# Kernel optimization log

Hardware: AMD Instinct MI355X
Metric: run time of the kernel (lower is better)

Reference implementation:

```python
import jax, jax.numpy as jnp
import numpy as np

N, E, F_IN, H, MH, C, G = 100000, 3200000, 128, 32, 64, 10, 64

def _seg_sum(data, ids, num):
    return jax.ops.segment_sum(data, ids, num_segments=num)

def gcn_conv(x, row, col, ew, W, b, n):
    # PyG GCNConv: linear first, then self-loops + symmetric edge-weight norm + scatter-add
    h = x @ W  # [N, H]
    loop = jnp.arange(n)
    r = jnp.concatenate([row, loop])
    c = jnp.concatenate([col, loop])
    w = jnp.concatenate([ew, jnp.ones((n,), dtype=ew.dtype)])
    deg = _seg_sum(w, c, n)
    dinv = jnp.where(deg > 0, jax.lax.rsqrt(deg), 0.0)
    norm = dinv[r] * w * dinv[c]  # [E+N]
    out = _seg_sum(norm[:, None] * h[r], c, n)  # scatter to targets
    return out + b

def setup_inputs():
    key = jax.random.key(0)
    ks = jax.random.split(key, 16)
    inp = {
        "x": jax.random.normal(ks[0], (N, F_IN), dtype=jnp.float32),
        "edge_index": jax.random.randint(ks[1], (2, E), 0, N, dtype=jnp.int64),
        "edge_weight": jax.random.uniform(ks[2], (E,), dtype=jnp.float32),
        "batch": jnp.sort(jax.random.randint(ks[3], (N,), 0, G, dtype=jnp.int64)),
    }
    def lin(k, i, o):
        s = 1.0 / np.sqrt(i)
        k1, k2 = jax.random.split(k)
        return (jax.random.uniform(k1, (i, o), minval=-s, maxval=s, dtype=jnp.float32),
                jax.random.uniform(k2, (o,), minval=-s, maxval=s, dtype=jnp.float32))
    inp["W1"], inp["b1"] = lin(ks[4], F_IN, H)
    inp["W2"], inp["b2"] = lin(ks[5], H, H)
    inp["W3"], inp["b3"] = lin(ks[6], H, H)
    inp["Wm0"], inp["bm0"] = lin(ks[7], H, MH)
    inp["Wm1"], inp["bm1"] = lin(ks[8], MH, MH)
    inp["Wout"], inp["bout"] = lin(ks[9], MH, C)
    return inp

def reference(x, edge_index, edge_weight, batch, W1, b1, W2, b2, W3, b3, Wm0, bm0, Wm1, bm1, Wout, bout):
    row, col = edge_index[0], edge_index[1]
    h = jax.nn.relu(gcn_conv(x, row, col, edge_weight, W1, b1, N))
    h = jax.nn.relu(gcn_conv(h, row, col, edge_weight, W2, b2, N))
    h = gcn_conv(h, row, col, edge_weight, W3, b3, N)
    # global mean pool over graphs
    sums = _seg_sum(h, batch, G)
    counts = _seg_sum(jnp.ones((N,), dtype=h.dtype), batch, G)
    g = sums / jnp.maximum(counts, 1.0)[:, None]
    # dropout p=0.5 is identity at inference (training=False)
    g = jax.nn.relu(g @ Wm0 + bm0)
    g = jax.nn.relu(g @ Wm1 + bm1)
    return g @ Wout + bout
```

## Files before the change

kernel.cpp:

```cpp
#include <hip/hip_runtime.h>

#define NN 100000
#define NE 3200000
#define FIN 128
#define HID 32
#define MH  64
#define NC  10
#define NG  64
#define NBKT 782
#define NBLK 512
#define EPB  (NE / NBLK)
#define SCANL (NBKT * NBLK)
#define SRCMASK 0x1FFFF
#define BCAP 5120

typedef float floatx2 __attribute__((ext_vector_type(2)));

__global__ __launch_bounds__(1024)
void hist_bkt(const int* __restrict__ ei, int* __restrict__ cnt2) {
    __shared__ int h[NBKT];
    int tid = threadIdx.x, blk = blockIdx.x;
    for (int b = tid; b < NBKT; b += 1024) h[b] = 0;
    __syncthreads();
    int base = blk * EPB;
    for (int i = tid; i < EPB; i += 1024)
        atomicAdd(&h[ei[NE + base + i] >> 7], 1);
    __syncthreads();
    for (int b = tid; b < NBKT; b += 1024) cnt2[b * NBLK + blk] = h[b];
}

__global__ void scan_block(const int* __restrict__ in, int* __restrict__ out,
                           int* __restrict__ bsum, int n) {
    __shared__ int lds[256];
    int tid = threadIdx.x;
    int base = blockIdx.x * 1024 + tid * 4;
    int v0 = 0, v1 = 0, v2 = 0, v3 = 0;
    if (base + 0 < n) v0 = in[base + 0];
    if (base + 1 < n) v1 = in[base + 1];
    if (base + 2 < n) v2 = in[base + 2];
    if (base + 3 < n) v3 = in[base + 3];
    int s = v0 + v1 + v2 + v3;
    lds[tid] = s;
    __syncthreads();
    for (int off = 1; off < 256; off <<= 1) {
        int val = (tid >= off) ? lds[tid - off] : 0;
        __syncthreads();
        lds[tid] += val;
        __syncthreads();
    }
    int excl = lds[tid] - s;
    if (tid == 255) bsum[blockIdx.x] = lds[255];
    if (base + 0 < n) out[base + 0] = excl;
    if (base + 1 < n) out[base + 1] = excl + v0;
    if (base + 2 < n) out[base + 2] = excl + v0 + v1;
    if (base + 3 < n) out[base + 3] = excl + v0 + v1 + v2;
}

__global__ void scan_top(int* __restrict__ bsum, int nb, float* __restrict__ sc) {
    int lane = threadIdx.x;
    for (int i = lane; i < NG * HID + NG; i += 64) sc[i] = 0.0f;
    int carry = 0;
    for (int base = 0; base < nb; base += 64) {
        int i = base + lane;
        int orig = (i < nb) ? bsum[i] : 0;
        int v = orig;
#pragma unroll
        for (int off = 1; off < 64; off <<= 1) {
            int t = __shfl_up(v, off, 64);
            if (lane >= off) v += t;
        }
        if (i < nb) bsum[i] = carry + v - orig;
        carry += __shfl(v, 63, 64);
    }
}

__global__ void scan_add(int* __restrict__ data, const int* __restrict__ bsum, int n) {
    int i = blockIdx.x * 256 + threadIdx.x;
    if (i < n) data[i] += bsum[i >> 10];
}

__global__ __launch_bounds__(1024)
void scatter_bkt(const int* __restrict__ ei, const float* __restrict__ ew,
                 const int* __restrict__ cnt2, const int* __restrict__ scanned,
                 int2* __restrict__ tre) {
    __shared__ int2 pay[EPB];
    __shared__ int scur[NBKT];
    __shared__ int hexc[NBKT];
    __shared__ int gbase[NBKT];
    int tid = threadIdx.x, blk = blockIdx.x;
    int myh = 0;
    if (tid < NBKT) {
        myh = cnt2[tid * NBLK + blk];
        gbase[tid] = scanned[tid * NBLK + blk];
        scur[tid] = myh;
    }
    __syncthreads();
    for (int off = 1; off < NBKT; off <<= 1) {
        int v = (tid < NBKT && tid >= off) ? scur[tid - off] : 0;
        __syncthreads();
        if (tid < NBKT) scur[tid] += v;
        __syncthreads();
    }
    if (tid < NBKT) { int ex = scur[tid] - myh; hexc[tid] = ex; scur[tid] = ex; }
    __syncthreads();
    int base = blk * EPB;
    for (int i = tid; i < EPB; i += 1024) {
        int e = base + i;
        int c = ei[NE + e];
        int r = ei[e];
        unsigned int wb = __float_as_uint(ew[e]);
        int b = c >> 7;
        int j = atomicAdd(&scur[b], 1);
        pay[j] = make_int2(r | ((c & 127) << 17) | ((b & 0xFF) << 24),
                           (int)((wb & ~3u) | ((unsigned)b >> 8)));
    }
    __syncthreads();
    for (int j = tid; j < EPB; j += 1024) {
        int2 q = pay[j];
        int b = (int)((((unsigned)q.y & 3u) << 8) | (((unsigned)q.x >> 24) & 0xFFu));
        int pos = gbase[b] + (j - hexc[b]);
        tre[pos] = make_int2(q.x & 0x00FFFFFF, q.y & ~3);
    }
}

__global__ __launch_bounds__(512)
void sort_k(const int2* __restrict__ tre, const int* __restrict__ scanned,
            unsigned int* __restrict__ srn4, int* __restrict__ rowptr,
            float* __restrict__ dinv) {
    __shared__ int2 ed[BCAP];
    __shared__ int h[128];
    __shared__ float dw[128];
    __shared__ int cur[128];
    int b = blockIdx.x, tid = threadIdx.x;
    int base = scanned[b * NBLK];
    int end = (b == NBKT - 1) ? NE : scanned[(b + 1) * NBLK];
    int n = end - base;
    bool staged = (n <= BCAP);
    if (tid < 128) { h[tid] = 0; dw[tid] = 0.f; }
    __syncthreads();
    for (int i = tid; i < n; i += 512) {
        int2 q = tre[base + i];
        if (staged) ed[i] = q;
        int key = (q.x >> 17) & 127;
        atomicAdd(&h[key], 1);
        atomicAdd(&dw[key], __int_as_float(q.y));
    }
    __syncthreads();
    if (tid < 64) {
        int lane = tid;
        int carry = 0;
#pragma unroll
        for (int c = 0; c < 2; ++c) {
            int idx = c * 64 + lane;
            int hv = h[idx];
            int v = hv;
#pragma unroll
            for (int off = 1; off < 64; off <<= 1) {
                int t = __shfl_up(v, off, 64);
                if (lane >= off) v += t;
            }
            cur[idx] = base + carry + v - hv;
            int node = b * 128 + idx;
            if (node < NN) {
                rowptr[node] = base + carry + v;
                dinv[node] = rsqrtf(1.0f + dw[idx]);
            }
            carry += __shfl(v, 63, 64);
        }
    }
    __syncthreads();
    for (int i = tid; i < n; i += 512) {
        int2 q = staged ? ed[i] : tre[base + i];
        int key = (q.x >> 17) & 127;
        int pos = atomicAdd(&cur[key], 1);
        unsigned int wb = (unsigned)q.y;
        wb += 0x7FFFu + ((wb >> 16) & 1u);
        srn4[pos] = (unsigned)(q.x & SRCMASK) | (((wb >> 16) & 0x7FFFu) << 17);
    }
}

template <int IN_DIM, bool RELU_IN>
__global__ __launch_bounds__(256)
void linear_k(const float* __restrict__ in, const float* __restrict__ W,
              const float* __restrict__ dinv, unsigned int* __restrict__ tmp8) {
    constexpr int J4 = IN_DIM / 4;
    constexpr int XSS = J4 + 1;
    __shared__ float4 xs[64 * XSS];
    __shared__ float4 wp[IN_DIM * 8];
    int tid = threadIdx.x;
    for (int idx = tid; idx < IN_DIM * 8; idx += 256) {
        int j = idx >> 3, kg = idx & 7;
        const float* wr = W + j * 32 + kg * 4;
        wp[idx] = make_float4(wr[0], wr[1], wr[2], wr[3]);
    }
    int rbase = blockIdx.x * 64;
    const float4* in4 = (const float4*)in;
    for (int idx = tid; idx < 64 * J4; idx += 256) {
        int row = idx / J4, j4 = idx % J4;
        int grow = rbase + row;
        float4 v = (grow < NN) ? in4[(size_t)grow * J4 + j4]
                               : make_float4(0.f, 0.f, 0.f, 0.f);
        if (RELU_IN) {
            v.x = fmaxf(v.x, 0.f); v.y = fmaxf(v.y, 0.f);
            v.z = fmaxf(v.z, 0.f); v.w = fmaxf(v.w, 0.f);
        }
        xs[row * XSS + j4] = v;
    }
    __syncthreads();
    int kg = tid & 7;
    int rp = tid >> 3;
    int r0 = rbase + 2 * rp;
    if (r0 >= NN) return;
    const float4* x0 = &xs[(2 * rp) * XSS];
    const float4* x1 = &xs[(2 * rp + 1) * XSS];
    float a00 = 0, a01 = 0, a02 = 0, a03 = 0;
    float a10 = 0, a11 = 0, a12 = 0, a13 = 0;
#pragma unroll
    for (int j4 = 0; j4 < J4; ++j4) {
        float4 v0 = x0[j4], v1 = x1[j4];
        const float4* wj = &wp[j4 * 4 * 8 + kg];
        float4 w0 = wj[0], w1 = wj[8], w2 = wj[16], w3 = wj[24];
#define LSTEP(VX0, VX1, W4) \
        a00 = fmaf(VX0, W4.x, a00); a01 = fmaf(VX0, W4.y, a01); \
        a02 = fmaf(VX0, W4.z, a02); a03 = fmaf(VX0, W4.w, a03); \
        a10 = fmaf(VX1, W4.x, a10); a11 = fmaf(VX1, W4.y, a11); \
        a12 = fmaf(VX1, W4.z, a12); a13 = fmaf(VX1, W4.w, a13);
        LSTEP(v0.x, v1.x, w0)
        LSTEP(v0.y, v1.y, w1)
        LSTEP(v0.z, v1.z, w2)
        LSTEP(v0.w, v1.w, w3)
#undef LSTEP
    }
    float d0 = dinv[r0], d1 = dinv[r0 + 1];
    a00 *= d0; a01 *= d0; a02 *= d0; a03 *= d0;
    a10 *= d1; a11 *= d1; a12 *= d1; a13 *= d1;
    int q0 = __builtin_amdgcn_cvt_pk_fp8_f32(a00, a01, 0, false);
    q0 = __builtin_amdgcn_cvt_pk_fp8_f32(a02, a03, q0, true);
    int q1 = __builtin_amdgcn_cvt_pk_fp8_f32(a10, a11, 0, false);
    q1 = __builtin_amdgcn_cvt_pk_fp8_f32(a12, a13, q1, true);
    tmp8[r0 * 8 + kg] = (unsigned int)q0;
    tmp8[(r0 + 1) * 8 + kg] = (unsigned int)q1;
}

#define AGG_BODY \
    int lane = threadIdx.x & 63; \
    int g = lane >> 3; \
    int q = lane & 7; \
    int end = rowptr[wid]; \
    int start = (wid == 0) ? 0 : rowptr[wid - 1]; \
    float a0 = 0, a1 = 0, a2 = 0, a3 = 0; \
    float b0 = 0, b1 = 0, b2 = 0, b3 = 0; \
    int e = start + g; \
    for (; e + 24 < end; e += 32) { \
        unsigned int p0 = srn4[e]; \
        unsigned int p1 = srn4[e + 8]; \
        unsigned int p2 = srn4[e + 16]; \
        unsigned int p3 = srn4[e + 24]; \
        unsigned int u0 = tmp8[(size_t)(p0 & SRCMASK) * 8 + q]; \
        unsigned int u1 = tmp8[(size_t)(p1 & SRCMASK) * 8 + q]; \
        unsigned int u2 = tmp8[(size_t)(p2 & SRCMASK) * 8 + q]; \
        unsigned int u3 = tmp8[(size_t)(p3 & SRCMASK) * 8 + q]; \
        float w0 = __uint_as_float((p0 >> 1) & 0x7FFF0000u); \
        float w1 = __uint_as_float((p1 >> 1) & 0x7FFF0000u); \
        float w2 = __uint_as_float((p2 >> 1) & 0x7FFF0000u); \
        float w3 = __uint_as_float((p3 >> 1) & 0x7FFF0000u); \
        floatx2 lo, hi; \
        lo = __builtin_amdgcn_cvt_pk_f32_fp8(u0, false); \
        hi = __builtin_amdgcn_cvt_pk_f32_fp8(u0, true); \
        a0 = fmaf(w0, lo.x, a0); a1 = fmaf(w0, lo.y, a1); \
        a2 = fmaf(w0, hi.x, a2); a3 = fmaf(w0, hi.y, a3); \
        lo = __builtin_amdgcn_cvt_pk_f32_fp8(u1, false); \
        hi = __builtin_amdgcn_cvt_pk_f32_fp8(u1, true); \
        b0 = fmaf(w1, lo.x, b0); b1 = fmaf(w1, lo.y, b1); \
        b2 = fmaf(w1, hi.x, b2); b3 = fmaf(w1, hi.y, b3); \
        lo = __builtin_amdgcn_cvt_pk_f32_fp8(u2, false); \
        hi = __builtin_amdgcn_cvt_pk_f32_fp8(u2, true); \
        a0 = fmaf(w2, lo.x, a0); a1 = fmaf(w2, lo.y, a1); \
        a2 = fmaf(w2, hi.x, a2); a3 = fmaf(w2, hi.y, a3); \
        lo = __builtin_amdgcn_cvt_pk_f32_fp8(u3, false); \
        hi = __builtin_amdgcn_cvt_pk_f32_fp8(u3, true); \
        b0 = fmaf(w3, lo.x, b0); b1 = fmaf(w3, lo.y, b1); \
        b2 = fmaf(w3, hi.x, b2); b3 = fmaf(w3, hi.y, b3); \
    } \
    for (; e < end; e += 8) { \
        unsigned int p = srn4[e]; \
        unsigned int u = tmp8[(size_t)(p & SRCMASK) * 8 + q]; \
        float w = __uint_as_float((p >> 1) & 0x7FFF0000u); \
        floatx2 lo = __builtin_amdgcn_cvt_pk_f32_fp8(u, false); \
        floatx2 hi = __builtin_amdgcn_cvt_pk_f32_fp8(u, true); \
        a0 = fmaf(w, lo.x, a0); a1 = fmaf(w, lo.y, a1); \
        a2 = fmaf(w, hi.x, a2); a3 = fmaf(w, hi.y, a3); \
    } \
    a0 += b0; a1 += b1; a2 += b2; a3 += b3; \
    a0 += __shfl_xor(a0, 8, 64); a1 += __shfl_xor(a1, 8, 64); \
    a2 += __shfl_xor(a2, 8, 64); a3 += __shfl_xor(a3, 8, 64); \
    a0 += __shfl_xor(a0, 16, 64); a1 += __shfl_xor(a1, 16, 64); \
    a2 += __shfl_xor(a2, 16, 64); a3 += __shfl_xor(a3, 16, 64); \
    a0 += __shfl_xor(a0, 32, 64); a1 += __shfl_xor(a1, 32, 64); \
    a2 += __shfl_xor(a2, 32, 64); a3 += __shfl_xor(a3, 32, 64);

__global__ void aggregate(const unsigned int* __restrict__ srn4,
                          const int* __restrict__ rowptr,
                          const float* __restrict__ dinv,
                          const float* __restrict__ bias,
                          const unsigned int* __restrict__ tmp8,
                          float* __restrict__ h) {
    int wid = (blockIdx.x * 256 + threadIdx.x) >> 6;
    if (wid >= NN) return;
    AGG_BODY
    if (g == 0) {
        float d = dinv[wid];
        unsigned int sv = tmp8[(size_t)wid * 8 + q];
        floatx2 slo = __builtin_amdgcn_cvt_pk_f32_fp8(sv, false);
        floatx2 shi = __builtin_amdgcn_cvt_pk_f32_fp8(sv, true);
        float4 bq = ((const float4*)bias)[q];
        float4 o;
        o.x = bq.x + d * (slo.x + a0);
        o.y = bq.y + d * (slo.y + a1);
        o.z = bq.z + d * (shi.x + a2);
        o.w = bq.w + d * (shi.y + a3);
        ((float4*)(h + (size_t)wid * HID))[q] = o;
    }
}

__global__ void agg_lin(const unsigned int* __restrict__ srn4,
                        const int* __restrict__ rowptr,
                        const float* __restrict__ dinv,
                        const float* __restrict__ bias,
                        const float* __restrict__ Wn,
                        const unsigned int* __restrict__ tmp8,
                        unsigned int* __restrict__ tmp8_out) {
    __shared__ float hrow[4][HID];
    int wid = (blockIdx.x * 256 + threadIdx.x) >> 6;
    if (wid >= NN) return;
    int wv = threadIdx.x >> 6;
    AGG_BODY
    float d = dinv[wid];
    if (g == 0) {
        unsigned int sv = tmp8[(size_t)wid * 8 + q];
        floatx2 slo = __builtin_amdgcn_cvt_pk_f32_fp8(sv, false);
        floatx2 shi = __builtin_amdgcn_cvt_pk_f32_fp8(sv, true);
        float4 bq = ((const float4*)bias)[q];
        float4 o;
        o.x = fmaxf(bq.x + d * (slo.x + a0), 0.f);
        o.y = fmaxf(bq.y + d * (slo.y + a1), 0.f);
        o.z = fmaxf(bq.z + d * (shi.x + a2), 0.f);
        o.w = fmaxf(bq.w + d * (shi.y + a3), 0.f);
        *((float4*)&hrow[wv][4 * q]) = o;
    }
    int j = lane & 31, half = lane >> 5;
    const float* hr = hrow[wv];
    const float* wc = Wn + j;
    float y = 0.f;
#pragma unroll
    for (int k = 0; k < 16; ++k) {
        int kk = half * 16 + k;
        y = fmaf(hr[kk], wc[kk * 32], y);
    }
    y += __shfl_xor(y, 32, 64);
    y *= d;
    float y1 = __shfl_down(y, 1, 64);
    float y2 = __shfl_down(y, 2, 64);
    float y3 = __shfl_down(y, 3, 64);
    if (half == 0 && (j & 3) == 0) {
        int w0 = __builtin_amdgcn_cvt_pk_fp8_f32(y, y1, 0, false);
        w0 = __builtin_amdgcn_cvt_pk_fp8_f32(y2, y3, w0, true);
        tmp8_out[wid * 8 + (j >> 2)] = (unsigned int)w0;
    }
}

__global__ void pool_k(const float* __restrict__ h, const int* __restrict__ batch,
                       float* __restrict__ sums, float* __restrict__ counts) {
    int t = blockIdx.x * 256 + threadIdx.x;
    int chunk = t >> 5, k = t & 31;
    int n0 = chunk * 32;
    if (n0 >= NN) return;
    int n1 = min(n0 + 32, NN);
    int g = batch[n0];
    float acc = 0.f, cacc = 0.f;
    for (int i = n0; i < n1; ++i) {
        int gi = batch[i];
        if (gi != g) {
            atomicAdd(&sums[g * HID + k], acc);
            if (k == 0) atomicAdd(&counts[g], cacc);
            g = gi; acc = 0.f; cacc = 0.f;
        }
        acc += h[(size_t)i * HID + k];
        cacc += 1.f;
    }
    atomicAdd(&sums[g * HID + k], acc);
    if (k == 0) atomicAdd(&counts[g], cacc);
}

__global__ __launch_bounds__(64)
void mlp_k(const float* __restrict__ sums, const float* __restrict__ counts,
           const float* __restrict__ Wm0, const float* __restrict__ bm0,
           const float* __restrict__ Wm1, const float* __restrict__ bm1,
           const float* __restrict__ Wout, const float* __restrict__ bout,
           float* __restrict__ out) {
    __shared__ float g0[HID];
    __shared__ float g1[MH];
    __shared__ float g2[MH];
    int g = blockIdx.x;
    int k = threadIdx.x;
    if (k < HID) g0[k] = sums[g * HID + k] / fmaxf(counts[g], 1.0f);
    __syncthreads();
    float acc = bm0[k];
#pragma unroll
    for (int j = 0; j < HID; ++j) acc = fmaf(g0[j], Wm0[j * MH + k], acc);
    g1[k] = fmaxf(acc, 0.f);
    __syncthreads();
    float acc2 = bm1[k];
#pragma unroll
    for (int j = 0; j < MH; ++j) acc2 = fmaf(g1[j], Wm1[j * MH + k], acc2);
    g2[k] = fmaxf(acc2, 0.f);
    __syncthreads();
    if (k < NC) {
        float acc3 = bout[k];
#pragma unroll
        for (int j = 0; j < MH; ++j) acc3 = fmaf(g2[j], Wout[j * NC + k], acc3);
        out[g * NC + k] = acc3;
    }
}

extern "C" void kernel_launch(void* const* d_in, const int* in_sizes, int n_in,
                              void* d_out, int out_size, void* d_ws, size_t ws_size,
                              hipStream_t stream) {
    const float* x    = (const float*)d_in[0];
    const int*   ei   = (const int*)d_in[1];
    const float* ew   = (const float*)d_in[2];
    const int*   batch= (const int*)d_in[3];
    const float* W1   = (const float*)d_in[4];
    const float* b1   = (const float*)d_in[5];
    const float* W2   = (const float*)d_in[6];
    const float* b2   = (const float*)d_in[7];
    const float* W3   = (const float*)d_in[8];
    const float* b3   = (const float*)d_in[9];
    const float* Wm0  = (const float*)d_in[10];
    const float* bm0  = (const float*)d_in[11];
    const float* Wm1  = (const float*)d_in[12];
    const float* bm1  = (const float*)d_in[13];
    const float* Wout = (const float*)d_in[14];
    const float* bout = (const float*)d_in[15];
    float* out = (float*)d_out;

    char* p = (char*)d_ws;
    unsigned int* srn4 = (unsigned int*)p; p += sizeof(unsigned int) * (size_t)NE;
    char*  S   = p;                      p += 12 * (size_t)NE;
    int2*  tre = (int2*)S;
    int*   cnt2    = (int*)(S + sizeof(int2) * (size_t)NE);
    int*   scanned = cnt2 + SCANL;
    unsigned int* tmp8  = (unsigned int*)S;
    unsigned int* tmp8b = tmp8 + (size_t)NN * 8;
    float* hA  = (float*)(S + 2 * (size_t)NN * HID);
    int*   bsum    = (int*)p;            p += sizeof(int) * 512;
    float* dinv    = (float*)p;          p += sizeof(float) * NN;
    int*   rowptr  = (int*)p;            p += sizeof(int) * NN;
    float* sums    = (float*)p;          p += sizeof(float) * NG * HID;
    float* counts  = (float*)p;

    dim3 blk(256);
    const int NB_SCAN = (SCANL + 1023) / 1024;
    const int NB_LIN = (NN + 63) / 64;

    hist_bkt<<<NBLK, 1024, 0, stream>>>(ei, cnt2);
    scan_block<<<NB_SCAN, blk, 0, stream>>>(cnt2, scanned, bsum, SCANL);
    scan_top<<<1, 64, 0, stream>>>(bsum, NB_SCAN, sums);
    scan_add<<<(SCANL + 255) / 256, blk, 0, stream>>>(scanned, bsum, SCANL);
    scatter_bkt<<<NBLK, 1024, 0, stream>>>(ei, ew, cnt2, scanned, tre);
    sort_k<<<NBKT, 512, 0, stream>>>(tre, scanned, srn4, rowptr, dinv);

    linear_k<FIN, false><<<NB_LIN, blk, 0, stream>>>(x, W1, dinv, tmp8);
    agg_lin<<<25000, blk, 0, stream>>>(srn4, rowptr, dinv, b1, W2, tmp8, tmp8b);
    agg_lin<<<25000, blk, 0, stream>>>(srn4, rowptr, dinv, b2, W3, tmp8b, tmp8);
    aggregate<<<25000, blk, 0, stream>>>(srn4, rowptr, dinv, b3, tmp8, hA);

    pool_k<<<391, blk, 0, stream>>>(hA, batch, sums, counts);
    mlp_k<<<NG, 64, 0, stream>>>(sums, counts, Wm0, bm0, Wm1, bm1, Wout, bout, out);
}
```

Before: 404.6 us.

## Fuse final aggregation with mean-pool and use packed float2 accumulation

Merges the last GCN aggregation with the global mean-pool kernel. Each block accumulates per-graph sums in shared memory when all four nodes share a graph, and otherwise does global atomics. This removes the hA write/read round trip and one launch. The aggregation core now uses packed float2 FMAs with byte-offset address math, and agg_lin loads its hidden row as float4 vectors. The trade-off is extra atomics and a block sync in the fused kernel.

After: 1.110 ms. 2.74x slower.

```diff
diff --git a/kernel.cpp b/kernel.cpp
--- a/kernel.cpp
+++ b/kernel.cpp
@@ -242,72 +242,84 @@
     tmp8[(r0 + 1) * 8 + kg] = (unsigned int)q1;
 }
 
-#define AGG_BODY \
-    int lane = threadIdx.x & 63; \
-    int g = lane >> 3; \
-    int q = lane & 7; \
-    int end = rowptr[wid]; \
-    int start = (wid == 0) ? 0 : rowptr[wid - 1]; \
-    float a0 = 0, a1 = 0, a2 = 0, a3 = 0; \
-    float b0 = 0, b1 = 0, b2 = 0, b3 = 0; \
-    int e = start + g; \
-    for (; e + 24 < end; e += 32) { \
-        unsigned int p0 = srn4[e]; \
-        unsigned int p1 = srn4[e + 8]; \
-        unsigned int p2 = srn4[e + 16]; \
-        unsigned int p3 = srn4[e + 24]; \
-        unsigned int u0 = tmp8[(size_t)(p0 & SRCMASK) * 8 + q]; \
-        unsigned int u1 = tmp8[(size_t)(p1 & SRCMASK) * 8 + q]; \
-        unsigned int u2 = tmp8[(size_t)(p2 & SRCMASK) * 8 + q]; \
-        unsigned int u3 = tmp8[(size_t)(p3 & SRCMASK) * 8 + q]; \
-        float w0 = __uint_as_float((p0 >> 1) & 0x7FFF0000u); \
-        float w1 = __uint_as_float((p1 >> 1) & 0x7FFF0000u); \
-        float w2 = __uint_as_float((p2 >> 1) & 0x7FFF0000u); \
-        float w3 = __uint_as_float((p3 >> 1) & 0x7FFF0000u); \
-        floatx2 lo, hi; \
-        lo = __builtin_amdgcn_cvt_pk_f32_fp8(u0, false); \
-        hi = __builtin_amdgcn_cvt_pk_f32_fp8(u0, true); \
-        a0 = fmaf(w0, lo.x, a0); a1 = fmaf(w0, lo.y, a1); \
-        a2 = fmaf(w0, hi.x, a2); a3 = fmaf(w0, hi.y, a3); \
-        lo = __builtin_amdgcn_cvt_pk_f32_fp8(u1, false); \
-        hi = __builtin_amdgcn_cvt_pk_f32_fp8(u1, true); \
-        b0 = fmaf(w1, lo.x, b0); b1 = fmaf(w1, lo.y, b1); \
-        b2 = fmaf(w1, hi.x, b2); b3 = fmaf(w1, hi.y, b3); \
-        lo = __builtin_amdgcn_cvt_pk_f32_fp8(u2, false); \
-        hi = __builtin_amdgcn_cvt_pk_f32_fp8(u2, true); \
-        a0 = fmaf(w2, lo.x, a0); a1 = fmaf(w2, lo.y, a1); \
-        a2 = fmaf(w2, hi.x, a2); a3 = fmaf(w2, hi.y, a3); \
-        lo = __builtin_amdgcn_cvt_pk_f32_fp8(u3, false); \
-        hi = __builtin_amdgcn_cvt_pk_f32_fp8(u3, true); \
-        b0 = fmaf(w3, lo.x, b0); b1 = fmaf(w3, lo.y, b1); \
-        b2 = fmaf(w3, hi.x, b2); b3 = fmaf(w3, hi.y, b3); \
-    } \
-    for (; e < end; e += 8) { \
-        unsigned int p = srn4[e]; \
-        unsigned int u = tmp8[(size_t)(p & SRCMASK) * 8 + q]; \
-        float w = __uint_as_float((p >> 1) & 0x7FFF0000u); \
-        floatx2 lo = __builtin_amdgcn_cvt_pk_f32_fp8(u, false); \
-        floatx2 hi = __builtin_amdgcn_cvt_pk_f32_fp8(u, true); \
-        a0 = fmaf(w, lo.x, a0); a1 = fmaf(w, lo.y, a1); \
-        a2 = fmaf(w, hi.x, a2); a3 = fmaf(w, hi.y, a3); \
-    } \
-    a0 += b0; a1 += b1; a2 += b2; a3 += b3; \
-    a0 += __shfl_xor(a0, 8, 64); a1 += __shfl_xor(a1, 8, 64); \
-    a2 += __shfl_xor(a2, 8, 64); a3 += __shfl_xor(a3, 8, 64); \
-    a0 += __shfl_xor(a0, 16, 64); a1 += __shfl_xor(a1, 16, 64); \
-    a2 += __shfl_xor(a2, 16, 64); a3 += __shfl_xor(a3, 16, 64); \
-    a0 += __shfl_xor(a0, 32, 64); a1 += __shfl_xor(a1, 32, 64); \
+__device__ __forceinline__ float4 agg_core(const unsigned int* __restrict__ srn4,
+                                           const int* __restrict__ rowptr,
+                                           const unsigned int* __restrict__ tmp8,
+                                           int wid, int g, int q) {
+    unsigned int qb = (unsigned int)q * 4u;
+    const char* t8 = (const char*)tmp8;
+    int end = rowptr[wid];
+    int start = (wid == 0) ? 0 : rowptr[wid - 1];
+    floatx2 a01 = {0.f, 0.f}, a23 = {0.f, 0.f};
+    floatx2 c01 = {0.f, 0.f}, c23 = {0.f, 0.f};
+    int e = start + g;
+    for (; e + 24 < end; e += 32) {
+        unsigned int p0 = srn4[e];
+        unsigned int p1 = srn4[e + 8];
+        unsigned int p2 = srn4[e + 16];
+        unsigned int p3 = srn4[e + 24];
+        unsigned int u0 = *(const unsigned int*)(t8 + (((p0 & SRCMASK) << 5) | qb));
+        unsigned int u1 = *(const unsigned int*)(t8 + (((p1 & SRCMASK) << 5) | qb));
+        unsigned int u2 = *(const unsigned int*)(t8 + (((p2 & SRCMASK) << 5) | qb));
+        unsigned int u3 = *(const unsigned int*)(t8 + (((p3 & SRCMASK) << 5) | qb));
+        float w0 = __uint_as_float((p0 >> 1) & 0x7FFF0000u);
+        float w1 = __uint_as_float((p1 >> 1) & 0x7FFF0000u);
+        float w2 = __uint_as_float((p2 >> 1) & 0x7FFF0000u);
+        float w3 = __uint_as_float((p3 >> 1) & 0x7FFF0000u);
+        floatx2 lo, hi;
+        lo = __builtin_amdgcn_cvt_pk_f32_fp8(u0, false);
+        hi = __builtin_amdgcn_cvt_pk_f32_fp8(u0, true);
+        a01 += lo * w0; a23 += hi * w0;
+        lo = __builtin_amdgcn_cvt_pk_f32_fp8(u1, false);
+        hi = __builtin_amdgcn_cvt_pk_f32_fp8(u1, true);
+        c01 += lo * w1; c23 += hi * w1;
+        lo = __builtin_amdgcn_cvt_pk_f32_fp8(u2, false);
+        hi = __builtin_amdgcn_cvt_pk_f32_fp8(u2, true);
+        a01 += lo * w2; a23 += hi * w2;
+        lo = __builtin_amdgcn_cvt_pk_f32_fp8(u3, false);
+        hi = __builtin_amdgcn_cvt_pk_f32_fp8(u3, true);
+        c01 += lo * w3; c23 += hi * w3;
+    }
+    for (; e < end; e += 8) {
+        unsigned int p = srn4[e];
+        unsigned int u = *(const unsigned int*)(t8 + (((p & SRCMASK) << 5) | qb));
+        float w = __uint_as_float((p >> 1) & 0x7FFF0000u);
+        floatx2 lo = __builtin_amdgcn_cvt_pk_f32_fp8(u, false);
+        floatx2 hi = __builtin_amdgcn_cvt_pk_f32_fp8(u, true);
+        a01 += lo * w; a23 += hi * w;
+    }
+    a01 += c01; a23 += c23;
+    float a0 = a01.x, a1 = a01.y, a2 = a23.x, a3 = a23.y;
+    a0 += __shfl_xor(a0, 8, 64);  a1 += __shfl_xor(a1, 8, 64);
+    a2 += __shfl_xor(a2, 8, 64);  a3 += __shfl_xor(a3, 8, 64);
+    a0 += __shfl_xor(a0, 16, 64); a1 += __shfl_xor(a1, 16, 64);
+    a2 += __shfl_xor(a2, 16, 64); a3 += __shfl_xor(a3, 16, 64);
+    a0 += __shfl_xor(a0, 32, 64); a1 += __shfl_xor(a1, 32, 64);
     a2 += __shfl_xor(a2, 32, 64); a3 += __shfl_xor(a3, 32, 64);
-
-__global__ void aggregate(const unsigned int* __restrict__ srn4,
-                          const int* __restrict__ rowptr,
-                          const float* __restrict__ dinv,
-                          const float* __restrict__ bias,
-                          const unsigned int* __restrict__ tmp8,
-                          float* __restrict__ h) {
-    int wid = (blockIdx.x * 256 + threadIdx.x) >> 6;
-    if (wid >= NN) return;
-    AGG_BODY
+    return make_float4(a0, a1, a2, a3);
+}
+
+__global__ __launch_bounds__(256)
+void agg_pool(const unsigned int* __restrict__ srn4,
+              const int* __restrict__ rowptr,
+              const float* __restrict__ dinv,
+              const float* __restrict__ bias,
+              const unsigned int* __restrict__ tmp8,
+              const int* __restrict__ batch,
+              float* __restrict__ sums, float* __restrict__ counts) {
+    __shared__ float psum[HID];
+    __shared__ int gids[4];
+    int tid = threadIdx.x;
+    int wid = (blockIdx.x * 256 + tid) >> 6;
+    int wv = tid >> 6;
+    int lane = tid & 63;
+    int g = lane >> 3, q = lane & 7;
+    int gid = batch[wid];
+    if (tid < HID) psum[tid] = 0.f;
+    if (lane == 0) gids[wv] = gid;
+    float4 a = agg_core(srn4, rowptr, tmp8, wid, g, q);
+    __syncthreads();
+    bool uni = (gids[0] == gids[3]);
     if (g == 0) {
         float d = dinv[wid];
         unsigned int sv = tmp8[(size_t)wid * 8 + q];
@@ -315,26 +327,42 @@
         floatx2 shi = __builtin_amdgcn_cvt_pk_f32_fp8(sv, true);
         float4 bq = ((const float4*)bias)[q];
         float4 o;
-        o.x = bq.x + d * (slo.x + a0);
-        o.y = bq.y + d * (slo.y + a1);
-        o.z = bq.z + d * (shi.x + a2);
-        o.w = bq.w + d * (shi.y + a3);
-        ((float4*)(h + (size_t)wid * HID))[q] = o;
-    }
-}
-
-__global__ void agg_lin(const unsigned int* __restrict__ srn4,
-                        const int* __restrict__ rowptr,
-                        const float* __restrict__ dinv,
-                        const float* __restrict__ bias,
-                        const float* __restrict__ Wn,
-                        const unsigned int* __restrict__ tmp8,
-                        unsigned int* __restrict__ tmp8_out) {
+        o.x = bq.x + d * (slo.x + a.x);
+        o.y = bq.y + d * (slo.y + a.y);
+        o.z = bq.z + d * (shi.x + a.z);
+        o.w = bq.w + d * (shi.y + a.w);
+        if (uni) {
+            atomicAdd(&psum[4 * q + 0], o.x);
+            atomicAdd(&psum[4 * q + 1], o.y);
+            atomicAdd(&psum[4 * q + 2], o.z);
+            atomicAdd(&psum[4 * q + 3], o.w);
+        } else {
+            atomicAdd(&sums[gid * HID + 4 * q + 0], o.x);
+            atomicAdd(&sums[gid * HID + 4 * q + 1], o.y);
+            atomicAdd(&sums[gid * HID + 4 * q + 2], o.z);
+            atomicAdd(&sums[gid * HID + 4 * q + 3], o.w);
+        }
+        if (lane == 0) atomicAdd(&counts[gid], 1.f);
+    }
+    __syncthreads();
+    if (uni && tid < HID) atomicAdd(&sums[gids[0] * HID + tid], psum[tid]);
+}
+
+__global__ __launch_bounds__(256)
+void agg_lin(const unsigned int* __restrict__ srn4,
+             const int* __restrict__ rowptr,
+             const float* __restrict__ dinv,
+             const float* __restrict__ bias,
+             const float* __restrict__ Wn,
+             const unsigned int* __restrict__ tmp8,
+             unsigned int* __restrict__ tmp8_out) {
     __shared__ float hrow[4][HID];
-    int wid = (blockIdx.x * 256 + threadIdx.x) >> 6;
-    if (wid >= NN) return;
-    int wv = threadIdx.x >> 6;
-    AGG_BODY
+    int tid = threadIdx.x;
+    int wid = (blockIdx.x * 256 + tid) >> 6;
+    int wv = tid >> 6;
+    int lane = tid & 63;
+    int g = lane >> 3, q = lane & 7;
+    float4 a = agg_core(srn4, rowptr, tmp8, wid, g, q);
     float d = dinv[wid];
     if (g == 0) {
         unsigned int sv = tmp8[(size_t)wid * 8 + q];
@@ -342,21 +370,23 @@
         floatx2 shi = __builtin_amdgcn_cvt_pk_f32_fp8(sv, true);
         float4 bq = ((const float4*)bias)[q];
         float4 o;
-        o.x = fmaxf(bq.x + d * (slo.x + a0), 0.f);
-        o.y = fmaxf(bq.y + d * (slo.y + a1), 0.f);
-        o.z = fmaxf(bq.z + d * (shi.x + a2), 0.f);
-        o.w = fmaxf(bq.w + d * (shi.y + a3), 0.f);
+        o.x = fmaxf(bq.x + d * (slo.x + a.x), 0.f);
+        o.y = fmaxf(bq.y + d * (slo.y + a.y), 0.f);
+        o.z = fmaxf(bq.z + d * (shi.x + a.z), 0.f);
+        o.w = fmaxf(bq.w + d * (shi.y + a.w), 0.f);
         *((float4*)&hrow[wv][4 * q]) = o;
     }
     int j = lane & 31, half = lane >> 5;
-    const float* hr = hrow[wv];
-    const float* wc = Wn + j;
+    const float4* h4 = (const float4*)&hrow[wv][half * 16];
+    float4 h0 = h4[0], h1 = h4[1], h2 = h4[2], h3 = h4[3];
+    float hh[16];
+    *((float4*)&hh[0]) = h0; *((float4*)&hh[4]) = h1;
+    *((float4*)&hh[8]) = h2; *((float4*)&hh[12]) = h3;
+    const float* wc = Wn + half * 16 * 32 + j;
     float y = 0.f;
 #pragma unroll
-    for (int k = 0; k < 16; ++k) {
-        int kk = half * 16 + k;
-        y = fmaf(hr[kk], wc[kk * 32], y);
-    }
+    for (int k = 0; k < 16; ++k)
+        y = fmaf(hh[k], wc[k * 32], y);
     y += __shfl_xor(y, 32, 64);
     y *= d;
     float y1 = __shfl_down(y, 1, 64);
@@ -367,29 +397,6 @@
         w0 = __builtin_amdgcn_cvt_pk_fp8_f32(y2, y3, w0, true);
         tmp8_out[wid * 8 + (j >> 2)] = (unsigned int)w0;
     }
-}
-
-__global__ void pool_k(const float* __restrict__ h, const int* __restrict__ batch,
-                       float* __restrict__ sums, float* __restrict__ counts) {
-    int t = blockIdx.x * 256 + threadIdx.x;
-    int chunk = t >> 5, k = t & 31;
-    int n0 = chunk * 32;
-    if (n0 >= NN) return;
-    int n1 = min(n0 + 32, NN);
-    int g = batch[n0];
-    float acc = 0.f, cacc = 0.f;
-    for (int i = n0; i < n1; ++i) {
-        int gi = batch[i];
-        if (gi != g) {
-            atomicAdd(&sums[g * HID + k], acc);
-            if (k == 0) atomicAdd(&counts[g], cacc);
-            g = gi; acc = 0.f; cacc = 0.f;
-        }
-        acc += h[(size_t)i * HID + k];
-        cacc += 1.f;
-    }
-    atomicAdd(&sums[g * HID + k], acc);
-    if (k == 0) atomicAdd(&counts[g], cacc);
 }
 
 __global__ __launch_bounds__(64)
@@ -452,7 +459,6 @@
     int*   scanned = cnt2 + SCANL;
     unsigned int* tmp8  = (unsigned int*)S;
     unsigned int* tmp8b = tmp8 + (size_t)NN * 8;
-    float* hA  = (float*)(S + 2 * (size_t)NN * HID);
     int*   bsum    = (int*)p;            p += sizeof(int) * 512;
     float* dinv    = (float*)p;          p += sizeof(float) * NN;
     int*   rowptr  = (int*)p;            p += sizeof(int) * NN;
@@ -473,8 +479,7 @@
     linear_k<FIN, false><<<NB_LIN, blk, 0, stream>>>(x, W1, dinv, tmp8);
     agg_lin<<<25000, blk, 0, stream>>>(srn4, rowptr, dinv, b1, W2, tmp8, tmp8b);
     agg_lin<<<25000, blk, 0, stream>>>(srn4, rowptr, dinv, b2, W3, tmp8b, tmp8);
-    aggregate<<<25000, blk, 0, stream>>>(srn4, rowptr, dinv, b3, tmp8, hA);
-
-    pool_k<<<391, blk, 0, stream>>>(hA, batch, sums, counts);
+    agg_pool<<<25000, blk, 0, stream>>>(srn4, rowptr, dinv, b3, tmp8, batch, sums, counts);
+
     mlp_k<<<NG, 64, 0, stream>>>(sums, counts, Wm0, bm0, Wm1, bm1, Wout, bout, out);
 }
```
